# Performance work log

Measured on AMD Instinct MI355X. Metric: run time of the kernel, lower is better.

## Reference

```python
import jax, jax.numpy as jnp
import numpy as np


def setup_inputs() -> dict:
    key = jax.random.key(0)
    k1, k2, k3, k4, k5 = jax.random.split(key, 5)
    b, t_q, t_k = 4, 256, 1024
    qs, ms, n = 512, 512, 128
    return {
        "query": jax.random.normal(k1, (b, t_q, qs), dtype=jnp.float32),
        "keys": jax.random.normal(k2, (b, t_k, ms), dtype=jnp.float32),
        "Wq": jax.random.normal(k3, (qs, n), dtype=jnp.float32) * 0.05,
        "Wk": jax.random.normal(k4, (ms, n), dtype=jnp.float32) * 0.05,
        "linear_att": jax.random.normal(k5, (n,), dtype=jnp.float32) * 0.05,
    }


def reference(query, keys, Wq, Wk, linear_att):
    # projections: b t_q n and b t_k n
    att_query = jnp.einsum("bqd,dn->bqn", query, Wq)
    att_keys = jnp.einsum("bkd,dn->bkn", keys, Wk)
    # Bahdanau additive score: tanh(q + k) . v  -> b t_q t_k
    sum_qk = att_query[:, :, None, :] + att_keys[:, None, :, :]
    scores = jnp.einsum("bqkn,n->bqk", jnp.tanh(sum_qk), linear_att)
    weights = jax.nn.softmax(scores, axis=-1)
    context = jnp.einsum("bqk,bkd->bqd", weights, keys)
    return (context, weights)
```

## Files before the change

kernel.cpp:

```cpp
#include <hip/hip_runtime.h>

#define B 4
#define TQ 256
#define TK 1024
#define QS 512
#define NN 128

#define TANH_SCALE 2.8853900817779268f
#define LOG2E 1.4426950408889634f
#define CTX_ELEMS ((size_t)B * TQ * QS)

__device__ __forceinline__ float fast_exp2(float x) {
#if __has_builtin(__builtin_amdgcn_exp2f)
    return __builtin_amdgcn_exp2f(x);
#else
    return exp2f(x);
#endif
}
__device__ __forceinline__ float fast_rcp(float x) {
#if __has_builtin(__builtin_amdgcn_rcpf)
    return __builtin_amdgcn_rcpf(x);
#else
    return 1.0f / x;
#endif
}

__global__ __launch_bounds__(256) void proj_kernel(
    const float* __restrict__ query, const float* __restrict__ keys,
    const float* __restrict__ Wq, const float* __restrict__ Wk,
    float* __restrict__ attq, float* __restrict__ attkT)
{
    __shared__ float As[32][9];
    __shared__ float Bs[32][132];

    const int tid = threadIdx.x;
    const int rb = blockIdx.x * 8;
    const bool isq = (rb < B * TQ);
    const float* A = isq ? (query + (size_t)rb * QS)
                         : (keys + (size_t)(rb - B * TQ) * QS);
    const float* W = isq ? Wq : Wk;

    const int n0 = (tid & 31) * 4;
    const int r  = tid >> 5;
    float acc[4] = {};

    for (int k0 = 0; k0 < QS; k0 += 32) {
        {
            const int rr = tid >> 5, c = tid & 31;
            As[c][rr] = A[(size_t)rr * QS + k0 + c];
        }
        {
            const int n = (tid & 31) * 4, r0 = tid >> 5;
            #pragma unroll
            for (int j = 0; j < 4; ++j) {
                const int kk = r0 + j * 8;
                *(float4*)&Bs[kk][n] =
                    *(const float4*)(W + (size_t)(k0 + kk) * NN + n);
            }
        }
        __syncthreads();
        #pragma unroll
        for (int kk = 0; kk < 32; ++kk) {
            const float a = As[kk][r];
            const float4 b = *(const float4*)&Bs[kk][n0];
            acc[0] = fmaf(a, b.x, acc[0]);
            acc[1] = fmaf(a, b.y, acc[1]);
            acc[2] = fmaf(a, b.z, acc[2]);
            acc[3] = fmaf(a, b.w, acc[3]);
        }
        __syncthreads();
    }

    if (isq) {
        float4 o;
        o.x = acc[0] * TANH_SCALE;
        o.y = acc[1] * TANH_SCALE;
        o.z = acc[2] * TANH_SCALE;
        o.w = acc[3] * TANH_SCALE;
        *(float4*)(attq + (size_t)(rb + r) * NN + n0) = o;
    } else {
        float4 o;
        o.x = acc[0] * TANH_SCALE;
        o.y = acc[1] * TANH_SCALE;
        o.z = acc[2] * TANH_SCALE;
        o.w = acc[3] * TANH_SCALE;
        *(float4*)&Bs[r][n0] = o;
        __syncthreads();
        const int rk = rb - B * TQ;
        const int bb = rk >> 10;
        const int kbase = rk & 1023;
        const int n = tid >> 1;
        const int kh = (tid & 1) * 4;
        float4 t;
        t.x = Bs[kh + 0][n];
        t.y = Bs[kh + 1][n];
        t.z = Bs[kh + 2][n];
        t.w = Bs[kh + 3][n];
        *(float4*)(attkT + (size_t)bb * NN * TK + (size_t)n * TK + kbase + kh) = t;
    }
}

__global__ __launch_bounds__(256) void score_softmax_kernel(
    const float* __restrict__ attq, const float* __restrict__ attkT,
    const float* __restrict__ vatt, float* __restrict__ wout)
{
    __shared__ float aqs[2][128];
    __shared__ float vsm[128];
    __shared__ float red[2][8];

    const int tid = threadIdx.x;
    const int b = blockIdx.x >> 7;
    const int q0 = (blockIdx.x & 127) * 2;

    if (tid < 128) {
        aqs[0][tid] = attq[((size_t)b * TQ + q0) * NN + tid];
        vsm[tid] = vatt[tid];
    } else {
        aqs[1][tid & 127] = attq[((size_t)b * TQ + q0 + 1) * NN + (tid & 127)];
    }
    __syncthreads();

    const float* kt = attkT + (size_t)b * NN * TK + (size_t)tid * 4;
    float s[2][4] = {};

    #pragma unroll 8
    for (int n = 0; n < 128; ++n) {
        const float4 a = *(const float4*)(kt + (size_t)n * TK);
        const float a0 = aqs[0][n], a1 = aqs[1][n], vv = vsm[n];
        const float av[4] = {a.x, a.y, a.z, a.w};
        #pragma unroll
        for (int rr = 0; rr < 4; ++rr) {
            const float x0 = a0 + av[rr];
            const float t0 = fmaf(-2.f, fast_rcp(1.f + fast_exp2(x0)), 1.f);
            s[0][rr] = fmaf(vv, t0, s[0][rr]);
            const float x1 = a1 + av[rr];
            const float t1 = fmaf(-2.f, fast_rcp(1.f + fast_exp2(x1)), 1.f);
            s[1][rr] = fmaf(vv, t1, s[1][rr]);
        }
    }

    const int lane = tid & 63, wid = tid >> 6;
    #pragma unroll
    for (int qq = 0; qq < 2; ++qq) {
        float mm = fmaxf(fmaxf(s[qq][0], s[qq][1]), fmaxf(s[qq][2], s[qq][3]));
        #pragma unroll
        for (int off = 32; off > 0; off >>= 1)
            mm = fmaxf(mm, __shfl_xor(mm, off, 64));
        if (lane == 0) red[qq][wid] = mm;
    }
    __syncthreads();
    float m[2];
    m[0] = fmaxf(fmaxf(red[0][0], red[0][1]), fmaxf(red[0][2], red[0][3]));
    m[1] = fmaxf(fmaxf(red[1][0], red[1][1]), fmaxf(red[1][2], red[1][3]));

    float e[2][4];
    #pragma unroll
    for (int qq = 0; qq < 2; ++qq) {
        float ls = 0.f;
        #pragma unroll
        for (int i = 0; i < 4; ++i) {
            e[qq][i] = fast_exp2((s[qq][i] - m[qq]) * LOG2E);
            ls += e[qq][i];
        }
        #pragma unroll
        for (int off = 32; off > 0; off >>= 1)
            ls += __shfl_xor(ls, off, 64);
        if (lane == 0) red[qq][4 + wid] = ls;
    }
    __syncthreads();
    #pragma unroll
    for (int qq = 0; qq < 2; ++qq) {
        const float S = red[qq][4] + red[qq][5] + red[qq][6] + red[qq][7];
        const float inv = fast_rcp(S);
        float4 w4;
        w4.x = e[qq][0] * inv; w4.y = e[qq][1] * inv;
        w4.z = e[qq][2] * inv; w4.w = e[qq][3] * inv;
        *(float4*)(wout + ((size_t)b * TQ + q0 + qq) * TK + (size_t)tid * 4) = w4;
    }
}

__global__ __launch_bounds__(256) void context_kernel(
    const float* __restrict__ keys, const float* __restrict__ w,
    float* __restrict__ ctx)
{
    __shared__ float Wst[32][17];
    __shared__ float Ks[32][64];

    const int tid = threadIdx.x;
    const int bid = blockIdx.x;
    const int b = bid >> 7;
    const int rem = bid & 127;
    const int qt = rem >> 3;
    const int dt = rem & 7;

    const float* wb = w + (size_t)b * TQ * TK + (size_t)qt * 16 * TK;
    const float* kb = keys + (size_t)b * TK * QS + dt * 64;

    const int d0 = (tid & 15) * 4;
    const int q  = tid >> 4;
    float acc[4] = {};

    for (int k0 = 0; k0 < TK; k0 += 32) {
        {
            const int rr = tid >> 4, c = (tid & 15) * 2;
            const float2 v = *(const float2*)(wb + (size_t)rr * TK + k0 + c);
            Wst[c + 0][rr] = v.x;
            Wst[c + 1][rr] = v.y;
        }
        {
            const int c = tid & 15, rr = tid >> 4;
            *(float4*)&Ks[rr][c * 4] =
                *(const float4*)(kb + (size_t)(k0 + rr) * QS + c * 4);
            *(float4*)&Ks[rr + 16][c * 4] =
                *(const float4*)(kb + (size_t)(k0 + rr + 16) * QS + c * 4);
        }
        __syncthreads();
        #pragma unroll
        for (int kk = 0; kk < 32; ++kk) {
            const float a = Wst[kk][q];
            const float4 bb = *(const float4*)&Ks[kk][d0];
            acc[0] = fmaf(a, bb.x, acc[0]);
            acc[1] = fmaf(a, bb.y, acc[1]);
            acc[2] = fmaf(a, bb.z, acc[2]);
            acc[3] = fmaf(a, bb.w, acc[3]);
        }
        __syncthreads();
    }

    float4 o;
    o.x = acc[0]; o.y = acc[1]; o.z = acc[2]; o.w = acc[3];
    *(float4*)(ctx + ((size_t)b * TQ + qt * 16 + q) * QS + dt * 64 + d0) = o;
}

extern "C" void kernel_launch(void* const* d_in, const int* in_sizes, int n_in,
                              void* d_out, int out_size, void* d_ws, size_t ws_size,
                              hipStream_t stream) {
    const float* query = (const float*)d_in[0];
    const float* keys  = (const float*)d_in[1];
    const float* Wq    = (const float*)d_in[2];
    const float* Wk    = (const float*)d_in[3];
    const float* vatt  = (const float*)d_in[4];

    float* ctx = (float*)d_out;
    float* wts = ctx + CTX_ELEMS;

    float* attq  = (float*)d_ws;
    float* attkT = attq + (size_t)B * TQ * NN;

    hipLaunchKernelGGL(proj_kernel, dim3((B * TQ + B * TK) / 8), dim3(256), 0,
                       stream, query, keys, Wq, Wk, attq, attkT);
    hipLaunchKernelGGL(score_softmax_kernel, dim3(B * TQ / 2), dim3(256), 0,
                       stream, attq, attkT, vatt, wts);
    hipLaunchKernelGGL(context_kernel, dim3(512), dim3(256), 0,
                       stream, keys, wts, ctx);
}
```

Baseline: 162.7 us.

## Factor tanh exponentials into projections and split-K the context GEMM

The projection kernel now stores exp2 of the scaled projections. The score loop can then use exp(q+k)=exp(q)*exp(k) and compute each tanh term as one FMA plus one reciprocal, with the -2v factor folded in and the constant v-sum term dropped because it cancels in softmax. The context kernel is restructured to use 4x4 register tiles and split the key dimension four ways, followed by a new reduce kernel over the partials in workspace. The exp factorisation can overflow to inf for large projections, and the split-K adds an extra launch plus the partial-buffer memory traffic.

Result: faster. 135.8 us (-16.5%).

```diff
diff --git a/kernel.cpp b/kernel.cpp
--- a/kernel.cpp
+++ b/kernel.cpp
@@ -71,19 +71,15 @@
         __syncthreads();
     }
 
+    float4 o;
+    o.x = fast_exp2(acc[0] * TANH_SCALE);
+    o.y = fast_exp2(acc[1] * TANH_SCALE);
+    o.z = fast_exp2(acc[2] * TANH_SCALE);
+    o.w = fast_exp2(acc[3] * TANH_SCALE);
+
     if (isq) {
-        float4 o;
-        o.x = acc[0] * TANH_SCALE;
-        o.y = acc[1] * TANH_SCALE;
-        o.z = acc[2] * TANH_SCALE;
-        o.w = acc[3] * TANH_SCALE;
         *(float4*)(attq + (size_t)(rb + r) * NN + n0) = o;
     } else {
-        float4 o;
-        o.x = acc[0] * TANH_SCALE;
-        o.y = acc[1] * TANH_SCALE;
-        o.z = acc[2] * TANH_SCALE;
-        o.w = acc[3] * TANH_SCALE;
         *(float4*)&Bs[r][n0] = o;
         __syncthreads();
         const int rk = rb - B * TQ;
@@ -104,8 +100,8 @@
     const float* __restrict__ attq, const float* __restrict__ attkT,
     const float* __restrict__ vatt, float* __restrict__ wout)
 {
-    __shared__ float aqs[2][128];
-    __shared__ float vsm[128];
+    __shared__ float eqs[2][128];
+    __shared__ float nv2[128];
     __shared__ float red[2][8];
 
     const int tid = threadIdx.x;
@@ -113,10 +109,10 @@
     const int q0 = (blockIdx.x & 127) * 2;
 
     if (tid < 128) {
-        aqs[0][tid] = attq[((size_t)b * TQ + q0) * NN + tid];
-        vsm[tid] = vatt[tid];
+        eqs[0][tid] = attq[((size_t)b * TQ + q0) * NN + tid];
+        nv2[tid] = -2.0f * vatt[tid];
     } else {
-        aqs[1][tid & 127] = attq[((size_t)b * TQ + q0 + 1) * NN + (tid & 127)];
+        eqs[1][tid & 127] = attq[((size_t)b * TQ + q0 + 1) * NN + (tid & 127)];
     }
     __syncthreads();
 
@@ -126,16 +122,14 @@
     #pragma unroll 8
     for (int n = 0; n < 128; ++n) {
         const float4 a = *(const float4*)(kt + (size_t)n * TK);
-        const float a0 = aqs[0][n], a1 = aqs[1][n], vv = vsm[n];
+        const float e0 = eqs[0][n], e1 = eqs[1][n], nv = nv2[n];
         const float av[4] = {a.x, a.y, a.z, a.w};
         #pragma unroll
         for (int rr = 0; rr < 4; ++rr) {
-            const float x0 = a0 + av[rr];
-            const float t0 = fmaf(-2.f, fast_rcp(1.f + fast_exp2(x0)), 1.f);
-            s[0][rr] = fmaf(vv, t0, s[0][rr]);
-            const float x1 = a1 + av[rr];
-            const float t1 = fmaf(-2.f, fast_rcp(1.f + fast_exp2(x1)), 1.f);
-            s[1][rr] = fmaf(vv, t1, s[1][rr]);
+            const float r0 = fast_rcp(fmaf(av[rr], e0, 1.0f));
+            s[0][rr] = fmaf(nv, r0, s[0][rr]);
+            const float r1 = fast_rcp(fmaf(av[rr], e1, 1.0f));
+            s[1][rr] = fmaf(nv, r1, s[1][rr]);
         }
     }
 
@@ -181,31 +175,37 @@
 
 __global__ __launch_bounds__(256) void context_kernel(
     const float* __restrict__ keys, const float* __restrict__ w,
-    float* __restrict__ ctx)
-{
-    __shared__ float Wst[32][17];
+    float* __restrict__ ctxp)
+{
+    __shared__ float Wst[32][66];
     __shared__ float Ks[32][64];
 
     const int tid = threadIdx.x;
     const int bid = blockIdx.x;
     const int b = bid >> 7;
     const int rem = bid & 127;
-    const int qt = rem >> 3;
-    const int dt = rem & 7;
-
-    const float* wb = w + (size_t)b * TQ * TK + (size_t)qt * 16 * TK;
-    const float* kb = keys + (size_t)b * TK * QS + dt * 64;
+    const int qt = rem >> 5;
+    const int dt = (rem >> 2) & 7;
+    const int ks = rem & 3;
+
+    const float* wb = w + (size_t)b * TQ * TK + (size_t)qt * 64 * TK + ks * 256;
+    const float* kb = keys + (size_t)b * TK * QS + (size_t)ks * 256 * QS + dt * 64;
 
     const int d0 = (tid & 15) * 4;
-    const int q  = tid >> 4;
-    float acc[4] = {};
-
-    for (int k0 = 0; k0 < TK; k0 += 32) {
-        {
-            const int rr = tid >> 4, c = (tid & 15) * 2;
-            const float2 v = *(const float2*)(wb + (size_t)rr * TK + k0 + c);
-            Wst[c + 0][rr] = v.x;
-            Wst[c + 1][rr] = v.y;
+    const int q0 = (tid >> 4) * 4;
+    float acc[4][4] = {};
+
+    const int wr = tid >> 2;
+    const int wc = (tid & 3) * 8;
+
+    for (int k0 = 0; k0 < 256; k0 += 32) {
+        {
+            const float4 v0 = *(const float4*)(wb + (size_t)wr * TK + k0 + wc);
+            const float4 v1 = *(const float4*)(wb + (size_t)wr * TK + k0 + wc + 4);
+            Wst[wc + 0][wr] = v0.x; Wst[wc + 1][wr] = v0.y;
+            Wst[wc + 2][wr] = v0.z; Wst[wc + 3][wr] = v0.w;
+            Wst[wc + 4][wr] = v1.x; Wst[wc + 5][wr] = v1.y;
+            Wst[wc + 6][wr] = v1.z; Wst[wc + 7][wr] = v1.w;
         }
         {
             const int c = tid & 15, rr = tid >> 4;
@@ -217,19 +217,46 @@
         __syncthreads();
         #pragma unroll
         for (int kk = 0; kk < 32; ++kk) {
-            const float a = Wst[kk][q];
+            const float2 a01 = *(const float2*)&Wst[kk][q0];
+            const float2 a23 = *(const float2*)&Wst[kk][q0 + 2];
             const float4 bb = *(const float4*)&Ks[kk][d0];
-            acc[0] = fmaf(a, bb.x, acc[0]);
-            acc[1] = fmaf(a, bb.y, acc[1]);
-            acc[2] = fmaf(a, bb.z, acc[2]);
-            acc[3] = fmaf(a, bb.w, acc[3]);
-        }
-        __syncthreads();
-    }
-
+            const float av[4] = {a01.x, a01.y, a23.x, a23.y};
+            #pragma unroll
+            for (int i = 0; i < 4; ++i) {
+                acc[i][0] = fmaf(av[i], bb.x, acc[i][0]);
+                acc[i][1] = fmaf(av[i], bb.y, acc[i][1]);
+                acc[i][2] = fmaf(av[i], bb.z, acc[i][2]);
+                acc[i][3] = fmaf(av[i], bb.w, acc[i][3]);
+            }
+        }
+        __syncthreads();
+    }
+
+    float* op = ctxp + (size_t)ks * CTX_ELEMS
+              + ((size_t)b * TQ + qt * 64 + q0) * QS + dt * 64 + d0;
+    #pragma unroll
+    for (int i = 0; i < 4; ++i) {
+        float4 o;
+        o.x = acc[i][0]; o.y = acc[i][1]; o.z = acc[i][2]; o.w = acc[i][3];
+        *(float4*)(op + (size_t)i * QS) = o;
+    }
+}
+
+__global__ __launch_bounds__(256) void reduce_kernel(
+    const float4* __restrict__ ctxp, float4* __restrict__ ctx)
+{
+    const size_t idx = (size_t)blockIdx.x * 256 + threadIdx.x;
+    const size_t stride = CTX_ELEMS / 4;
+    const float4 a = ctxp[idx];
+    const float4 b = ctxp[idx + stride];
+    const float4 c = ctxp[idx + 2 * stride];
+    const float4 d = ctxp[idx + 3 * stride];
     float4 o;
-    o.x = acc[0]; o.y = acc[1]; o.z = acc[2]; o.w = acc[3];
-    *(float4*)(ctx + ((size_t)b * TQ + qt * 16 + q) * QS + dt * 64 + d0) = o;
+    o.x = (a.x + b.x) + (c.x + d.x);
+    o.y = (a.y + b.y) + (c.y + d.y);
+    o.z = (a.z + b.z) + (c.z + d.z);
+    o.w = (a.w + b.w) + (c.w + d.w);
+    ctx[idx] = o;
 }
 
 extern "C" void kernel_launch(void* const* d_in, const int* in_sizes, int n_in,
@@ -246,11 +273,14 @@
 
     float* attq  = (float*)d_ws;
     float* attkT = attq + (size_t)B * TQ * NN;
+    float* ctxp  = attkT + (size_t)B * NN * TK;
 
     hipLaunchKernelGGL(proj_kernel, dim3((B * TQ + B * TK) / 8), dim3(256), 0,
                        stream, query, keys, Wq, Wk, attq, attkT);
     hipLaunchKernelGGL(score_softmax_kernel, dim3(B * TQ / 2), dim3(256), 0,
                        stream, attq, attkT, vatt, wts);
     hipLaunchKernelGGL(context_kernel, dim3(512), dim3(256), 0,
-                       stream, keys, wts, ctx);
-}
+                       stream, keys, wts, ctxp);
+    hipLaunchKernelGGL(reduce_kernel, dim3((unsigned)(CTX_ELEMS / 4 / 256)), dim3(256), 0,
+                       stream, (const float4*)ctxp, (float4*)ctx);
+}
```
